# Performance work log

Hardware: AMD Instinct MI355X
Metric: run time of the kernel (lower is better)

Reference implementation:

```python
import jax, jax.numpy as jnp
import numpy as np

INPUT_DIM, DIM, N_ACTIONS = 2048, 1024, 64
B, T = 1024, 16

def setup_inputs() -> dict:
    key = jax.random.key(0)
    ks = jax.random.split(key, 8)
    s = 1.0 / np.sqrt(INPUT_DIM)
    return {
        "precondition": jax.random.normal(ks[0], (B, T, INPUT_DIM), jnp.float32),
        "effect": jax.random.normal(ks[1], (B, T, INPUT_DIM), jnp.float32),
        "action": jax.random.randint(ks[2], (B,), 0, N_ACTIONS, jnp.int32),
        "Wp": jax.random.uniform(ks[3], (DIM, INPUT_DIM), jnp.float32, -s, s),
        "bp": jax.random.uniform(ks[4], (DIM,), jnp.float32, -s, s),
        "We": jax.random.uniform(ks[5], (DIM, INPUT_DIM), jnp.float32, -s, s),
        "be": jax.random.uniform(ks[6], (DIM,), jnp.float32, -s, s),
        "W_trans": jax.random.normal(ks[7], (N_ACTIONS, DIM, DIM), jnp.float32) * 0.02,
    }

def reference(precondition, effect, action, Wp, bp, We, be, W_trans):
    # mean-pool over time
    p_avg = precondition.mean(axis=1)  # [B, input_dim]
    e_avg = effect.mean(axis=1)        # [B, input_dim]
    # linear projections
    p_embed = p_avg @ Wp.T + bp        # [B, dim]
    e_embed = e_avg @ We.T + be        # [B, dim]
    # gather per-sample transformation matrix, then batched matvec
    sel = W_trans[action]              # [B, dim, dim]
    p_t = jnp.einsum('bij,bj->bi', sel, p_embed)  # [B, dim]
    # torch: bmm(...).unsqueeze(1) on [B, dim, 1] -> [B, 1, dim, 1]
    p_transformed = p_t[:, None, :, None]
    return (p_transformed, e_embed)
```

## Files before the change

kernel.cpp:

```cpp
#include <hip/hip_runtime.h>
#include <stdint.h>

#define IDIM 2048
#define ODIM 1024
#define NACT 64
#define NB 1024
#define NT 16

typedef __attribute__((ext_vector_type(8))) short short8;
typedef __attribute__((ext_vector_type(4))) float floatx4;

__device__ __forceinline__ unsigned short f2bf(float f) {
    union { float f; unsigned u; } v; v.f = f;
    unsigned r = v.u + 0x7FFFu + ((v.u >> 16) & 1u);
    return (unsigned short)(r >> 16);
}

__global__ __launch_bounds__(256) void k_avg(const float* __restrict__ p,
                                             const float* __restrict__ e,
                                             unsigned short* __restrict__ pavg,
                                             unsigned short* __restrict__ eavg) {
    int idx = blockIdx.x * 256 + threadIdx.x;
    int b  = idx >> 9;
    int d4 = idx & 511;
    const float4* pr = (const float4*)(p + (size_t)b * (NT * IDIM)) + d4;
    const float4* er = (const float4*)(e + (size_t)b * (NT * IDIM)) + d4;
    float sx=0, sy=0, sz=0, sw=0, tx=0, ty=0, tz=0, tw=0;
#pragma unroll
    for (int t = 0; t < NT; ++t) {
        float4 a = pr[t * (IDIM/4)];
        float4 c = er[t * (IDIM/4)];
        sx += a.x; sy += a.y; sz += a.z; sw += a.w;
        tx += c.x; ty += c.y; tz += c.z; tw += c.w;
    }
    const float s = 1.0f / NT;
    ushort4 op = make_ushort4(f2bf(sx*s), f2bf(sy*s), f2bf(sz*s), f2bf(sw*s));
    ushort4 oe = make_ushort4(f2bf(tx*s), f2bf(ty*s), f2bf(tz*s), f2bf(tw*s));
    *(ushort4*)(pavg + (size_t)b*IDIM + d4*4) = op;
    *(ushort4*)(eavg + (size_t)b*IDIM + d4*4) = oe;
}

__global__ __launch_bounds__(256) void k_cvt(const float* __restrict__ w,
                                             unsigned short* __restrict__ o) {
    int idx = blockIdx.x * 256 + threadIdx.x;
    float4 v = ((const float4*)w)[idx];
    *(ushort4*)(o + (size_t)idx*4) = make_ushort4(f2bf(v.x), f2bf(v.y), f2bf(v.z), f2bf(v.w));
}

__global__ void k_group(const int* __restrict__ action,
                        int* __restrict__ order, int* __restrict__ starts) {
    __shared__ int cnt[NACT], cnt2[NACT], base[NACT];
    int t = threadIdx.x;
    if (t < NACT) { cnt[t] = 0; cnt2[t] = 0; }
    __syncthreads();
    int a = action[t];
    atomicAdd(&cnt[a], 1);
    __syncthreads();
    if (t < NACT) {
        int s = 0;
        for (int j = 0; j < t; ++j) s += cnt[j];
        base[t] = s;
        starts[t] = s;
        if (t == NACT - 1) starts[NACT] = s + cnt[t];
    }
    __syncthreads();
    int pos = base[a] + atomicAdd(&cnt2[a], 1);
    order[pos] = t;
}

__global__ __launch_bounds__(256) void k_embed(const unsigned short* __restrict__ pavg,
                                               const unsigned short* __restrict__ eavg,
                                               const unsigned short* __restrict__ wpb,
                                               const unsigned short* __restrict__ web,
                                               const float* __restrict__ bp,
                                               const float* __restrict__ be,
                                               unsigned short* __restrict__ peb,
                                               float* __restrict__ eout) {
    const int z = blockIdx.z;
    const unsigned short* Ag = z ? eavg : pavg;
    const unsigned short* Wg = z ? web  : wpb;
    const float* bias        = z ? be   : bp;
    const int row0 = blockIdx.x * 128;
    const int col0 = blockIdx.y * 64;
    __shared__ unsigned short As[128*40];
    __shared__ unsigned short Bs[64*40];
    const int tid  = threadIdx.x;
    const int w    = tid >> 6, lane = tid & 63;
    const int lr   = lane & 15, quad = lane >> 4;
    floatx4 acc[2][4];
#pragma unroll
    for (int s = 0; s < 2; ++s)
#pragma unroll
        for (int t = 0; t < 4; ++t) { floatx4 zz = {0.f,0.f,0.f,0.f}; acc[s][t] = zz; }

    const int rA0 = tid >> 2,        pA0 = tid & 3;
    const int rA1 = (tid+256) >> 2,  pA1 = tid & 3;

    for (int ks = 0; ks < IDIM/32; ++ks) {
        const int k0 = ks * 32;
        int4 a0 = *(const int4*)(Ag + (size_t)(row0 + rA0)*IDIM + k0 + pA0*8);
        int4 a1 = *(const int4*)(Ag + (size_t)(row0 + rA1)*IDIM + k0 + pA1*8);
        int4 b0 = *(const int4*)(Wg + (size_t)(col0 + rA0)*IDIM + k0 + pA0*8);
        __syncthreads();
        *(int4*)(&As[rA0*40 + pA0*8]) = a0;
        *(int4*)(&As[rA1*40 + pA1*8]) = a1;
        *(int4*)(&Bs[rA0*40 + pA0*8]) = b0;
        __syncthreads();
        short8 af[2], bf[4];
#pragma unroll
        for (int s = 0; s < 2; ++s)
            af[s] = *(const short8*)&As[(w*32 + s*16 + lr)*40 + quad*8];
#pragma unroll
        for (int t = 0; t < 4; ++t)
            bf[t] = *(const short8*)&Bs[(t*16 + lr)*40 + quad*8];
#pragma unroll
        for (int s = 0; s < 2; ++s)
#pragma unroll
            for (int t = 0; t < 4; ++t)
                acc[s][t] = __builtin_amdgcn_mfma_f32_16x16x32_bf16(af[s], bf[t], acc[s][t], 0, 0, 0);
    }

#pragma unroll
    for (int s = 0; s < 2; ++s) {
        const int rg = row0 + w*32 + s*16 + quad*4;
#pragma unroll
        for (int t = 0; t < 4; ++t) {
            const int cg = col0 + t*16 + lr;
            const float bv = bias[cg];
#pragma unroll
            for (int r = 0; r < 4; ++r) {
                float val = acc[s][t][r] + bv;
                if (z) eout[(size_t)(rg + r)*ODIM + cg] = val;
                else   peb[(size_t)(rg + r)*ODIM + cg] = f2bf(val);
            }
        }
    }
}

__global__ __launch_bounds__(256) void k_trans(const float* __restrict__ Wt,
                                               const unsigned short* __restrict__ peb,
                                               const int* __restrict__ order,
                                               const int* __restrict__ starts,
                                               float* __restrict__ out) {
    const int a  = blockIdx.z;
    const int g0 = starts[a], g1 = starts[a+1];
    const int gs = g0 + blockIdx.y * 32;
    int nb = g1 - gs;
    if (nb <= 0) return;
    if (nb > 32) nb = 32;
    const int i0 = blockIdx.x * 128;
    const float* M = Wt + (size_t)a * ODIM * ODIM;
    __shared__ unsigned short Ms[128*40];
    __shared__ unsigned short Ps[32*40];
    __shared__ int sorder[32];
    const int tid = threadIdx.x;
    if (tid < 32) sorder[tid] = order[gs + (tid < nb ? tid : 0)];
    __syncthreads();
    const int w  = tid >> 6, lane = tid & 63;
    const int lr = lane & 15, quad = lane >> 4;
    const int prw = sorder[(tid >> 2) & 31];
    floatx4 acc[2][2];
#pragma unroll
    for (int s = 0; s < 2; ++s)
#pragma unroll
        for (int t = 0; t < 2; ++t) { floatx4 zz = {0.f,0.f,0.f,0.f}; acc[s][t] = zz; }

    for (int ks = 0; ks < ODIM/32; ++ks) {
        const int k0 = ks * 32;
        float4 mv[4];
#pragma unroll
        for (int u = 0; u < 4; ++u) {
            int c = tid + u*256;
            int r = c >> 3, pt = c & 7;
            mv[u] = *(const float4*)(M + (size_t)(i0 + r)*ODIM + k0 + pt*4);
        }
        int4 pv;
        if (tid < 128) {
            int pt = tid & 3;
            pv = *(const int4*)(peb + (size_t)prw*ODIM + k0 + pt*8);
        }
        __syncthreads();
#pragma unroll
        for (int u = 0; u < 4; ++u) {
            int c = tid + u*256;
            int r = c >> 3, pt = c & 7;
            *(ushort4*)(&Ms[r*40 + pt*4]) =
                make_ushort4(f2bf(mv[u].x), f2bf(mv[u].y), f2bf(mv[u].z), f2bf(mv[u].w));
        }
        if (tid < 128) {
            int r = tid >> 2, pt = tid & 3;
            *(int4*)(&Ps[r*40 + pt*8]) = pv;
        }
        __syncthreads();
        short8 af[2], bf[2];
#pragma unroll
        for (int s = 0; s < 2; ++s)
            af[s] = *(const short8*)&Ms[(w*32 + s*16 + lr)*40 + quad*8];
#pragma unroll
        for (int t = 0; t < 2; ++t)
            bf[t] = *(const short8*)&Ps[(t*16 + lr)*40 + quad*8];
#pragma unroll
        for (int s = 0; s < 2; ++s)
#pragma unroll
            for (int t = 0; t < 2; ++t)
                acc[s][t] = __builtin_amdgcn_mfma_f32_16x16x32_bf16(af[s], bf[t], acc[s][t], 0, 0, 0);
    }

#pragma unroll
    for (int t = 0; t < 2; ++t) {
        int bb = t*16 + lr;
        if (bb < nb) {
            int bg = sorder[bb];
#pragma unroll
            for (int s = 0; s < 2; ++s) {
                int ig = i0 + w*32 + s*16 + quad*4;
                float4 v = make_float4(acc[s][t][0], acc[s][t][1], acc[s][t][2], acc[s][t][3]);
                *(float4*)(out + (size_t)bg*ODIM + ig) = v;
            }
        }
    }
}

extern "C" void kernel_launch(void* const* d_in, const int* in_sizes, int n_in,
                              void* d_out, int out_size, void* d_ws, size_t ws_size,
                              hipStream_t stream) {
    const float* prec = (const float*)d_in[0];
    const float* eff  = (const float*)d_in[1];
    const int*   act  = (const int*)d_in[2];
    const float* Wp   = (const float*)d_in[3];
    const float* bp   = (const float*)d_in[4];
    const float* We   = (const float*)d_in[5];
    const float* be   = (const float*)d_in[6];
    const float* Wt   = (const float*)d_in[7];
    float* out = (float*)d_out;

    uint8_t* ws = (uint8_t*)d_ws;
    unsigned short* pavg = (unsigned short*)(ws + 0);
    unsigned short* eavg = (unsigned short*)(ws + 4194304);
    unsigned short* wpb  = (unsigned short*)(ws + 8388608);
    unsigned short* web  = (unsigned short*)(ws + 12582912);
    unsigned short* peb  = (unsigned short*)(ws + 16777216);
    int* order  = (int*)(ws + 18874368);
    int* starts = order + NB;

    hipLaunchKernelGGL(k_avg,   dim3(2048),     dim3(256),  0, stream, prec, eff, pavg, eavg);
    hipLaunchKernelGGL(k_cvt,   dim3(2048),     dim3(256),  0, stream, Wp, wpb);
    hipLaunchKernelGGL(k_cvt,   dim3(2048),     dim3(256),  0, stream, We, web);
    hipLaunchKernelGGL(k_group, dim3(1),        dim3(1024), 0, stream, act, order, starts);
    hipLaunchKernelGGL(k_embed, dim3(8,16,2),   dim3(256),  0, stream,
                       pavg, eavg, wpb, web, bp, be, peb, out + 1048576);
    hipLaunchKernelGGL(k_trans, dim3(8,32,64),  dim3(256),  0, stream,
                       Wt, peb, order, starts, out);
}
```

Before: 621.5 us.

## Fuse weight bf16 conversion into embed GEMM and halve trans row tile

Removes the two separate fp32-to-bf16 conversion kernels for Wp and We. k_embed now loads the fp32 weights directly and converts them while staging into shared memory. This saves two launches and a round trip of the converted weights through memory, but each embed block now reads fp32 weights redundantly across the row-tiles. Separately, k_trans uses a 64-row tile instead of 128, doubling the grid to add parallelism, at the cost of rereading the P tile twice as often.

```diff
diff --git a/kernel.cpp b/kernel.cpp
--- a/kernel.cpp
+++ b/kernel.cpp
@@ -40,13 +40,6 @@
     *(ushort4*)(eavg + (size_t)b*IDIM + d4*4) = oe;
 }
 
-__global__ __launch_bounds__(256) void k_cvt(const float* __restrict__ w,
-                                             unsigned short* __restrict__ o) {
-    int idx = blockIdx.x * 256 + threadIdx.x;
-    float4 v = ((const float4*)w)[idx];
-    *(ushort4*)(o + (size_t)idx*4) = make_ushort4(f2bf(v.x), f2bf(v.y), f2bf(v.z), f2bf(v.w));
-}
-
 __global__ void k_group(const int* __restrict__ action,
                         int* __restrict__ order, int* __restrict__ starts) {
     __shared__ int cnt[NACT], cnt2[NACT], base[NACT];
@@ -70,15 +63,15 @@
 
 __global__ __launch_bounds__(256) void k_embed(const unsigned short* __restrict__ pavg,
                                                const unsigned short* __restrict__ eavg,
-                                               const unsigned short* __restrict__ wpb,
-                                               const unsigned short* __restrict__ web,
+                                               const float* __restrict__ Wpg,
+                                               const float* __restrict__ Weg,
                                                const float* __restrict__ bp,
                                                const float* __restrict__ be,
                                                unsigned short* __restrict__ peb,
                                                float* __restrict__ eout) {
     const int z = blockIdx.z;
     const unsigned short* Ag = z ? eavg : pavg;
-    const unsigned short* Wg = z ? web  : wpb;
+    const float* Wg          = z ? Weg  : Wpg;
     const float* bias        = z ? be   : bp;
     const int row0 = blockIdx.x * 128;
     const int col0 = blockIdx.y * 64;
@@ -93,18 +86,22 @@
 #pragma unroll
         for (int t = 0; t < 4; ++t) { floatx4 zz = {0.f,0.f,0.f,0.f}; acc[s][t] = zz; }
 
-    const int rA0 = tid >> 2,        pA0 = tid & 3;
-    const int rA1 = (tid+256) >> 2,  pA1 = tid & 3;
+    const int rA0 = tid >> 2,       pA0 = tid & 3;
+    const int rA1 = (tid+256) >> 2;
+    const int rW0 = tid >> 3,       pW0 = tid & 7;
+    const int rW1 = (tid+256) >> 3;
 
     for (int ks = 0; ks < IDIM/32; ++ks) {
         const int k0 = ks * 32;
         int4 a0 = *(const int4*)(Ag + (size_t)(row0 + rA0)*IDIM + k0 + pA0*8);
-        int4 a1 = *(const int4*)(Ag + (size_t)(row0 + rA1)*IDIM + k0 + pA1*8);
-        int4 b0 = *(const int4*)(Wg + (size_t)(col0 + rA0)*IDIM + k0 + pA0*8);
+        int4 a1 = *(const int4*)(Ag + (size_t)(row0 + rA1)*IDIM + k0 + pA0*8);
+        float4 w0 = *(const float4*)(Wg + (size_t)(col0 + rW0)*IDIM + k0 + pW0*4);
+        float4 w1 = *(const float4*)(Wg + (size_t)(col0 + rW1)*IDIM + k0 + pW0*4);
         __syncthreads();
         *(int4*)(&As[rA0*40 + pA0*8]) = a0;
-        *(int4*)(&As[rA1*40 + pA1*8]) = a1;
-        *(int4*)(&Bs[rA0*40 + pA0*8]) = b0;
+        *(int4*)(&As[rA1*40 + pA0*8]) = a1;
+        *(ushort4*)(&Bs[rW0*40 + pW0*4]) = make_ushort4(f2bf(w0.x), f2bf(w0.y), f2bf(w0.z), f2bf(w0.w));
+        *(ushort4*)(&Bs[rW1*40 + pW0*4]) = make_ushort4(f2bf(w1.x), f2bf(w1.y), f2bf(w1.z), f2bf(w1.w));
         __syncthreads();
         short8 af[2], bf[4];
 #pragma unroll
@@ -148,9 +145,9 @@
     int nb = g1 - gs;
     if (nb <= 0) return;
     if (nb > 32) nb = 32;
-    const int i0 = blockIdx.x * 128;
+    const int i0 = blockIdx.x * 64;
     const float* M = Wt + (size_t)a * ODIM * ODIM;
-    __shared__ unsigned short Ms[128*40];
+    __shared__ unsigned short Ms[64*40];
     __shared__ unsigned short Ps[32*40];
     __shared__ int sorder[32];
     const int tid = threadIdx.x;
@@ -159,51 +156,36 @@
     const int w  = tid >> 6, lane = tid & 63;
     const int lr = lane & 15, quad = lane >> 4;
     const int prw = sorder[(tid >> 2) & 31];
-    floatx4 acc[2][2];
-#pragma unroll
-    for (int s = 0; s < 2; ++s)
-#pragma unroll
-        for (int t = 0; t < 2; ++t) { floatx4 zz = {0.f,0.f,0.f,0.f}; acc[s][t] = zz; }
+    const int rM0 = tid >> 3,       pM0 = tid & 7;
+    const int rM1 = (tid+256) >> 3;
+    floatx4 acc[2];
+    { floatx4 zz = {0.f,0.f,0.f,0.f}; acc[0] = zz; acc[1] = zz; }
 
     for (int ks = 0; ks < ODIM/32; ++ks) {
         const int k0 = ks * 32;
-        float4 mv[4];
-#pragma unroll
-        for (int u = 0; u < 4; ++u) {
-            int c = tid + u*256;
-            int r = c >> 3, pt = c & 7;
-            mv[u] = *(const float4*)(M + (size_t)(i0 + r)*ODIM + k0 + pt*4);
-        }
+        float4 m0 = *(const float4*)(M + (size_t)(i0 + rM0)*ODIM + k0 + pM0*4);
+        float4 m1 = *(const float4*)(M + (size_t)(i0 + rM1)*ODIM + k0 + pM0*4);
         int4 pv;
         if (tid < 128) {
             int pt = tid & 3;
             pv = *(const int4*)(peb + (size_t)prw*ODIM + k0 + pt*8);
         }
         __syncthreads();
-#pragma unroll
-        for (int u = 0; u < 4; ++u) {
-            int c = tid + u*256;
-            int r = c >> 3, pt = c & 7;
-            *(ushort4*)(&Ms[r*40 + pt*4]) =
-                make_ushort4(f2bf(mv[u].x), f2bf(mv[u].y), f2bf(mv[u].z), f2bf(mv[u].w));
-        }
+        *(ushort4*)(&Ms[rM0*40 + pM0*4]) = make_ushort4(f2bf(m0.x), f2bf(m0.y), f2bf(m0.z), f2bf(m0.w));
+        *(ushort4*)(&Ms[rM1*40 + pM0*4]) = make_ushort4(f2bf(m1.x), f2bf(m1.y), f2bf(m1.z), f2bf(m1.w));
         if (tid < 128) {
             int r = tid >> 2, pt = tid & 3;
             *(int4*)(&Ps[r*40 + pt*8]) = pv;
         }
         __syncthreads();
-        short8 af[2], bf[2];
-#pragma unroll
-        for (int s = 0; s < 2; ++s)
-            af[s] = *(const short8*)&Ms[(w*32 + s*16 + lr)*40 + quad*8];
+        short8 af, bf[2];
+        af = *(const short8*)&Ms[(w*16 + lr)*40 + quad*8];
 #pragma unroll
         for (int t = 0; t < 2; ++t)
             bf[t] = *(const short8*)&Ps[(t*16 + lr)*40 + quad*8];
 #pragma unroll
-        for (int s = 0; s < 2; ++s)
-#pragma unroll
-            for (int t = 0; t < 2; ++t)
-                acc[s][t] = __builtin_amdgcn_mfma_f32_16x16x32_bf16(af[s], bf[t], acc[s][t], 0, 0, 0);
+        for (int t = 0; t < 2; ++t)
+            acc[t] = __builtin_amdgcn_mfma_f32_16x16x32_bf16(af, bf[t], acc[t], 0, 0, 0);
     }
 
 #pragma unroll
@@ -211,12 +193,9 @@
         int bb = t*16 + lr;
         if (bb < nb) {
             int bg = sorder[bb];
-#pragma unroll
-            for (int s = 0; s < 2; ++s) {
-                int ig = i0 + w*32 + s*16 + quad*4;
-                float4 v = make_float4(acc[s][t][0], acc[s][t][1], acc[s][t][2], acc[s][t][3]);
-                *(float4*)(out + (size_t)bg*ODIM + ig) = v;
-            }
+            int ig = i0 + w*16 + quad*4;
+            float4 v = make_float4(acc[t][0], acc[t][1], acc[t][2], acc[t][3]);
+            *(float4*)(out + (size_t)bg*ODIM + ig) = v;
         }
     }
 }
@@ -237,18 +216,14 @@
     uint8_t* ws = (uint8_t*)d_ws;
     unsigned short* pavg = (unsigned short*)(ws + 0);
     unsigned short* eavg = (unsigned short*)(ws + 4194304);
-    unsigned short* wpb  = (unsigned short*)(ws + 8388608);
-    unsigned short* web  = (unsigned short*)(ws + 12582912);
-    unsigned short* peb  = (unsigned short*)(ws + 16777216);
-    int* order  = (int*)(ws + 18874368);
+    unsigned short* peb  = (unsigned short*)(ws + 8388608);
+    int* order  = (int*)(ws + 10485760);
     int* starts = order + NB;
 
     hipLaunchKernelGGL(k_avg,   dim3(2048),     dim3(256),  0, stream, prec, eff, pavg, eavg);
-    hipLaunchKernelGGL(k_cvt,   dim3(2048),     dim3(256),  0, stream, Wp, wpb);
-    hipLaunchKernelGGL(k_cvt,   dim3(2048),     dim3(256),  0, stream, We, web);
     hipLaunchKernelGGL(k_group, dim3(1),        dim3(1024), 0, stream, act, order, starts);
     hipLaunchKernelGGL(k_embed, dim3(8,16,2),   dim3(256),  0, stream,
-                       pavg, eavg, wpb, web, bp, be, peb, out + 1048576);
-    hipLaunchKernelGGL(k_trans, dim3(8,32,64),  dim3(256),  0, stream,
+                       pavg, eavg, Wp, We, bp, be, peb, out + 1048576);
+    hipLaunchKernelGGL(k_trans, dim3(16,32,64), dim3(256),  0, stream,
                        Wt, peb, order, starts, out);
 }
```

After: 624.1 us. Within noise of the previous version (+0.4%).
